# Optimization experiments

Measured on AMD Instinct MI355X. Metric: run time of the kernel, lower is better.

Reference implementation:

```python
import jax, jax.numpy as jnp
import numpy as np

N_NODES = 100000
N_EDGES = 1_600_000
IN_DIM, HID, OUT_DIM, N_BLOCKS = 963, 192, 3, 6


def spmm(src, dst, w, x):
    # sparse adj @ x, adj[dst, src] = w  (COO edge list)
    msgs = x[src] * w[:, None]                      # [E, F]
    return jax.ops.segment_sum(msgs, dst, num_segments=N_NODES)


def gconv(x, src, dst, ew, w, lw, b):
    # Pixel2Mesh GConv: adj @ (x @ W) + x @ W_loop + b
    return spmm(src, dst, ew, x @ w) + x @ lw + b


def setup_inputs() -> dict:
    key = jax.random.key(0)
    ks = jax.random.split(key, 13)
    s = 0.02  # small init scale to keep deep stack numerically tame
    return {
        "inputs": jax.random.normal(ks[0], (N_NODES, IN_DIM), jnp.float32),
        "edge_src": jax.random.randint(ks[1], (N_EDGES,), 0, N_NODES),
        "edge_dst": jax.random.randint(ks[2], (N_EDGES,), 0, N_NODES),
        "edge_weight": jax.random.uniform(ks[3], (N_EDGES,), jnp.float32) / 16.0,
        "w_in": jax.random.normal(ks[4], (IN_DIM, HID), jnp.float32) * s,
        "loop_in": jax.random.normal(ks[5], (IN_DIM, HID), jnp.float32) * s,
        "b_in": jnp.zeros((HID,), jnp.float32),
        "blocks_w": jax.random.normal(ks[6], (N_BLOCKS, 2, HID, HID), jnp.float32) * s,
        "blocks_loop": jax.random.normal(ks[7], (N_BLOCKS, 2, HID, HID), jnp.float32) * s,
        "blocks_b": jnp.zeros((N_BLOCKS, 2, HID), jnp.float32),
        "w_out": jax.random.normal(ks[8], (HID, OUT_DIM), jnp.float32) * s,
        "loop_out": jax.random.normal(ks[9], (HID, OUT_DIM), jnp.float32) * s,
        "b_out": jnp.zeros((OUT_DIM,), jnp.float32),
    }


def reference(inputs, edge_src, edge_dst, edge_weight, w_in, loop_in, b_in,
              blocks_w, blocks_loop, blocks_b, w_out, loop_out, b_out):
    x = gconv(inputs, edge_src, edge_dst, edge_weight, w_in, loop_in, b_in)

    def block(x, params):
        bw, bl, bb = params
        h = gconv(x, edge_src, edge_dst, edge_weight, bw[0], bl[0], bb[0])
        h = gconv(h, edge_src, edge_dst, edge_weight, bw[1], bl[1], bb[1])
        return (x + h) * 0.5, None

    x_cat, _ = jax.lax.scan(block, x, (blocks_w, blocks_loop, blocks_b))
    x_out = gconv(x_cat, edge_src, edge_dst, edge_weight, w_out, loop_out, b_out)
    return (x_out, x_cat)
```

## Files before the change

kernel.cpp:

```cpp
#include <hip/hip_runtime.h>
#include <cstdint>
#include <cstddef>

#define N_NODES 100000
#define N_EDGES 1600000
#define IN_DIM 963
#define HID 192
#define OUT_DIM 3

typedef _Float16 f16x8 __attribute__((ext_vector_type(8)));
typedef _Float16 f16x4 __attribute__((ext_vector_type(4)));
typedef float f32x4 __attribute__((ext_vector_type(4)));

__global__ void count_kernel(const int* __restrict__ dst, int* __restrict__ counts, int E) {
    int i = blockIdx.x * blockDim.x + threadIdx.x;
    if (i < E) atomicAdd(&counts[dst[i]], 1);
}

__global__ void scan_kernel(const int* __restrict__ counts, int* __restrict__ row_ptr, int n) {
    __shared__ int buf[1024];
    __shared__ int carry_s;
    int t = threadIdx.x;
    if (t == 0) { carry_s = 0; row_ptr[0] = 0; }
    __syncthreads();
    for (int base = 0; base < n; base += 1024) {
        int idx = base + t;
        int v = (idx < n) ? counts[idx] : 0;
        buf[t] = v;
        __syncthreads();
        for (int off = 1; off < 1024; off <<= 1) {
            int add = (t >= off) ? buf[t - off] : 0;
            __syncthreads();
            buf[t] += add;
            __syncthreads();
        }
        int carry = carry_s;
        if (idx < n) row_ptr[idx + 1] = carry + buf[t];
        __syncthreads();
        if (t == 1023) carry_s = carry + buf[1023];
        __syncthreads();
    }
}

__global__ void copy_cursor_kernel(const int* __restrict__ rp, int* __restrict__ cursor, int n) {
    int i = blockIdx.x * blockDim.x + threadIdx.x;
    if (i < n) cursor[i] = rp[i];
}

__global__ void scatter_kernel(const int* __restrict__ src, const int* __restrict__ dst,
                               const float* __restrict__ w, int* __restrict__ cursor,
                               int* __restrict__ csr_src, float* __restrict__ csr_w,
                               int* __restrict__ csr_eid, int E) {
    int i = blockIdx.x * blockDim.x + threadIdx.x;
    if (i < E) {
        int d = dst[i];
        int p = atomicAdd(&cursor[d], 1);
        csr_src[p] = src[i];
        csr_w[p] = w[i];
        csr_eid[p] = i;
    }
}

__global__ void sortrow_kernel(const int* __restrict__ rp, int* __restrict__ csr_src,
                               float* __restrict__ csr_w, int* __restrict__ csr_eid, int n) {
    int r = blockIdx.x * blockDim.x + threadIdx.x;
    if (r >= n) return;
    int s = rp[r], e = rp[r + 1];
    for (int i = s + 1; i < e; ++i) {
        int ke = csr_eid[i]; int ks = csr_src[i]; float kw = csr_w[i];
        int j = i - 1;
        while (j >= s && csr_eid[j] > ke) {
            csr_eid[j + 1] = csr_eid[j];
            csr_src[j + 1] = csr_src[j];
            csr_w[j + 1] = csr_w[j];
            --j;
        }
        csr_eid[j + 1] = ke; csr_src[j + 1] = ks; csr_w[j + 1] = kw;
    }
}

__global__ __launch_bounds__(256)
void trans_split(const float* __restrict__ W, const float* __restrict__ L,
                 int K, int Kp, _Float16* __restrict__ out_hi, _Float16* __restrict__ out_lo) {
    __shared__ float tile[32][33];
    const int n0 = blockIdx.x * 32, k0 = blockIdx.y * 32;
    const int tx = threadIdx.x, ty = threadIdx.y;
#pragma unroll
    for (int i = 0; i < 4; ++i) {
        int k = k0 + ty + i * 8;
        int n = n0 + tx;
        float v = 0.f;
        if (k < K) v = (n < HID) ? W[(size_t)k * HID + n] : L[(size_t)k * HID + (n - HID)];
        tile[ty + i * 8][tx] = v;
    }
    __syncthreads();
#pragma unroll
    for (int i = 0; i < 4; ++i) {
        int nl = ty + i * 8;
        int n = n0 + nl;
        int k = k0 + tx;
        float v = tile[tx][nl];
        _Float16 hi = (_Float16)v;
        _Float16 lo = (_Float16)(v - (float)hi);
        out_hi[(size_t)n * Kp + k] = hi;
        out_lo[(size_t)n * Kp + k] = lo;
    }
}

__global__ __launch_bounds__(256, 2)
void gemm_mfma(const float* __restrict__ X, int M, int Kx, int Kp,
               const _Float16* __restrict__ Wth, const _Float16* __restrict__ Wtl,
               const float* __restrict__ bias, const float* __restrict__ res,
               float* __restrict__ Hdst, float* __restrict__ Tdst) {
    __shared__ __align__(16) _Float16 Ah[4096];
    __shared__ __align__(16) _Float16 Al[4096];
    __shared__ __align__(16) _Float16 Bh[4096];
    __shared__ __align__(16) _Float16 Bl[4096];

    const int m0 = blockIdx.x * 128;
    const int bcol = blockIdx.y * 128;
    const int tid = threadIdx.x;
    const int lane = tid & 63;
    const int wave = tid >> 6;
    const int wr = wave >> 1, wc = wave & 1;

    const int sr = tid >> 1;
    const int sh = tid & 1;
    const int arow = m0 + sr;
    const bool arok = arow < M;
    const float* xrow = X + (size_t)(arok ? arow : 0) * Kx;

    const int bnl_lo = tid >> 2;
    const int bq = tid & 3;

    f32x4 pa[4];
    f16x8 pb[4];

    auto loadA = [&](int k0) {
        if (arok && (k0 + 32) <= Kx) {
            const float* p = xrow + k0 + sh * 16;
            pa[0] = *(const f32x4*)(p);
            pa[1] = *(const f32x4*)(p + 4);
            pa[2] = *(const f32x4*)(p + 8);
            pa[3] = *(const f32x4*)(p + 12);
        } else {
#pragma unroll
            for (int c = 0; c < 4; ++c) {
                f32x4 v = {0.f, 0.f, 0.f, 0.f};
#pragma unroll
                for (int j = 0; j < 4; ++j) {
                    int k = k0 + sh * 16 + c * 4 + j;
                    if (arok && k < Kx) v[j] = xrow[k];
                }
                pa[c] = v;
            }
        }
    };
    auto loadB = [&](int k0) {
#pragma unroll
        for (int it = 0; it < 4; ++it) {
            const _Float16* srcp = (it < 2) ? Wth : Wtl;
            int nl = (it & 1) * 64 + bnl_lo;
            pb[it] = *(const f16x8*)(srcp + (size_t)(bcol + nl) * Kp + k0 + bq * 8);
        }
    };
    auto stashA = [&]() {
#pragma unroll
        for (int c = 0; c < 2; ++c) {
            f16x8 hi, lo;
#pragma unroll
            for (int j = 0; j < 8; ++j) {
                int e = c * 8 + j;
                float x = pa[e >> 2][e & 3];
                _Float16 h = (_Float16)x;
                hi[j] = h;
                lo[j] = (_Float16)(x - (float)h);
            }
            int kg = sh * 2 + c;
            int off = (sr >> 4) * 512 + kg * 128 + ((sr & 15) ^ kg) * 8;
            *(f16x8*)&Ah[off] = hi;
            *(f16x8*)&Al[off] = lo;
        }
    };
    auto stashB = [&]() {
#pragma unroll
        for (int it = 0; it < 4; ++it) {
            int nl = (it & 1) * 64 + bnl_lo;
            int off = (nl >> 4) * 512 + bq * 128 + ((nl & 15) ^ bq) * 8;
            _Float16* dst = (it < 2) ? Bh : Bl;
            *(f16x8*)&dst[off] = pb[it];
        }
    };

    f32x4 acc[4][4];
#pragma unroll
    for (int i = 0; i < 4; ++i)
#pragma unroll
        for (int j = 0; j < 4; ++j)
            acc[i][j] = f32x4{0.f, 0.f, 0.f, 0.f};

    const int lro = (lane >> 4) * 128 + ((lane & 15) ^ (lane >> 4)) * 8;

    loadA(0); loadB(0);
    for (int k0 = 0; k0 < Kx; k0 += 32) {
        stashA(); stashB();
        __syncthreads();
        if (k0 + 32 < Kx) { loadA(k0 + 32); loadB(k0 + 32); }
        f16x8 ah[4], al[4], bh[4], bl[4];
#pragma unroll
        for (int i = 0; i < 4; ++i) {
            ah[i] = *(const f16x8*)&Ah[(wr * 4 + i) * 512 + lro];
            al[i] = *(const f16x8*)&Al[(wr * 4 + i) * 512 + lro];
            bh[i] = *(const f16x8*)&Bh[(wc * 4 + i) * 512 + lro];
            bl[i] = *(const f16x8*)&Bl[(wc * 4 + i) * 512 + lro];
        }
#pragma unroll
        for (int mi = 0; mi < 4; ++mi)
#pragma unroll
            for (int ni = 0; ni < 4; ++ni) {
                acc[mi][ni] = __builtin_amdgcn_mfma_f32_16x16x32_f16(ah[mi], bh[ni], acc[mi][ni], 0, 0, 0);
                acc[mi][ni] = __builtin_amdgcn_mfma_f32_16x16x32_f16(al[mi], bh[ni], acc[mi][ni], 0, 0, 0);
                acc[mi][ni] = __builtin_amdgcn_mfma_f32_16x16x32_f16(ah[mi], bl[ni], acc[mi][ni], 0, 0, 0);
            }
        __syncthreads();
    }

#pragma unroll
    for (int mi = 0; mi < 4; ++mi) {
        int rbase = m0 + wr * 64 + mi * 16 + ((lane >> 4) << 2);
#pragma unroll
        for (int ni = 0; ni < 4; ++ni) {
            int gc = bcol + wc * 64 + ni * 16 + (lane & 15);
            f32x4 v = acc[mi][ni];
            if (gc < HID) {
#pragma unroll
                for (int j = 0; j < 4; ++j) {
                    int row = rbase + j;
                    if (row < M) Hdst[(size_t)row * HID + gc] = v[j];
                }
            } else {
                int c = gc - HID;
                float bv = bias[c];
#pragma unroll
                for (int j = 0; j < 4; ++j) {
                    int row = rbase + j;
                    if (row < M) {
                        float t = v[j] + bv;
                        if (res != nullptr) t += res[(size_t)row * HID + c];
                        Tdst[(size_t)row * HID + c] = t;
                    }
                }
            }
        }
    }
}

__global__ __launch_bounds__(256)
void spmm_kernel(const int* __restrict__ rp, const int* __restrict__ csrc,
                 const float* __restrict__ cw, const float* __restrict__ Hm,
                 float* __restrict__ out, float scale) {
    int wid = (blockIdx.x * 256 + threadIdx.x) >> 6;
    int lane = threadIdx.x & 63;
    if (wid >= N_NODES) return;
    int s = rp[wid], e = rp[wid + 1];
    float a0 = 0.f, a1 = 0.f, a2 = 0.f;
    int i = s;
    for (; i + 1 < e; i += 2) {
        float w0 = cw[i], w1 = cw[i + 1];
        const float* h0 = Hm + (size_t)csrc[i] * HID;
        const float* h1 = Hm + (size_t)csrc[i + 1] * HID;
        float x00 = h0[lane], x01 = h0[64 + lane], x02 = h0[128 + lane];
        float x10 = h1[lane], x11 = h1[64 + lane], x12 = h1[128 + lane];
        a0 += w0 * x00; a1 += w0 * x01; a2 += w0 * x02;
        a0 += w1 * x10; a1 += w1 * x11; a2 += w1 * x12;
    }
    if (i < e) {
        float w = cw[i];
        const float* h = Hm + (size_t)csrc[i] * HID;
        a0 += w * h[lane];
        a1 += w * h[64 + lane];
        a2 += w * h[128 + lane];
    }
    float* o = out + (size_t)wid * HID;
    o[lane]       = scale * (o[lane] + a0);
    o[64 + lane]  = scale * (o[64 + lane] + a1);
    o[128 + lane] = scale * (o[128 + lane] + a2);
}

__global__ __launch_bounds__(256)
void out_gemm(const float* __restrict__ X, const float* __restrict__ Wout,
              const float* __restrict__ Lout, const float* __restrict__ bout,
              float* __restrict__ H3, float* __restrict__ T3) {
    __shared__ float Ws[HID * OUT_DIM];
    __shared__ float Ls[HID * OUT_DIM];
    int tid = threadIdx.x;
    for (int i = tid; i < HID * OUT_DIM; i += 256) { Ws[i] = Wout[i]; Ls[i] = Lout[i]; }
    __syncthreads();
    int n = blockIdx.x * 4 + (tid >> 6);
    int lane = tid & 63;
    if (n >= N_NODES) return;
    const float* x = X + (size_t)n * HID;
    float aw[3] = {0.f, 0.f, 0.f}, al[3] = {0.f, 0.f, 0.f};
#pragma unroll
    for (int p = 0; p < 3; ++p) {
        int k = p * 64 + lane;
        float xv = x[k];
#pragma unroll
        for (int c = 0; c < 3; ++c) {
            aw[c] += xv * Ws[k * 3 + c];
            al[c] += xv * Ls[k * 3 + c];
        }
    }
#pragma unroll
    for (int off = 32; off > 0; off >>= 1) {
#pragma unroll
        for (int c = 0; c < 3; ++c) {
            aw[c] += __shfl_down(aw[c], off, 64);
            al[c] += __shfl_down(al[c], off, 64);
        }
    }
    if (lane == 0) {
#pragma unroll
        for (int c = 0; c < 3; ++c) {
            H3[n * 3 + c] = aw[c];
            T3[n * 3 + c] = al[c] + bout[c];
        }
    }
}

__global__ __launch_bounds__(256)
void out_spmm(const int* __restrict__ rp, const int* __restrict__ csrc,
              const float* __restrict__ cw, const float* __restrict__ H3,
              const float* __restrict__ T3, float* __restrict__ out) {
    int n = blockIdx.x * blockDim.x + threadIdx.x;
    if (n >= N_NODES) return;
    int s = rp[n], e = rp[n + 1];
    float a0 = 0.f, a1 = 0.f, a2 = 0.f;
    for (int i = s; i < e; ++i) {
        float w = cw[i];
        int src = csrc[i];
        a0 += w * H3[src * 3 + 0];
        a1 += w * H3[src * 3 + 1];
        a2 += w * H3[src * 3 + 2];
    }
    out[n * 3 + 0] = a0 + T3[n * 3 + 0];
    out[n * 3 + 1] = a1 + T3[n * 3 + 1];
    out[n * 3 + 2] = a2 + T3[n * 3 + 2];
}

extern "C" void kernel_launch(void* const* d_in, const int* in_sizes, int n_in,
                              void* d_out, int out_size, void* d_ws, size_t ws_size,
                              hipStream_t stream) {
    const float* X0    = (const float*)d_in[0];
    const int*   esrc  = (const int*)d_in[1];
    const int*   edst  = (const int*)d_in[2];
    const float* ew    = (const float*)d_in[3];
    const float* w_in  = (const float*)d_in[4];
    const float* l_in  = (const float*)d_in[5];
    const float* b_in  = (const float*)d_in[6];
    const float* bw    = (const float*)d_in[7];
    const float* bl    = (const float*)d_in[8];
    const float* bb    = (const float*)d_in[9];
    const float* w_out = (const float*)d_in[10];
    const float* l_out = (const float*)d_in[11];
    const float* b_out = (const float*)d_in[12];

    char* ws = (char*)d_ws;
    size_t off = 0;
    auto alloc = [&](size_t bytes) -> void* {
        void* p = ws + off;
        off += (bytes + 255) & ~(size_t)255;
        return p;
    };
    float* Hbuf   = (float*)alloc(sizeof(float) * (size_t)N_NODES * HID);
    float* h1     = (float*)alloc(sizeof(float) * (size_t)N_NODES * HID);
    int*   counts = (int*)alloc(sizeof(int) * N_NODES);
    int*   rp     = (int*)alloc(sizeof(int) * (N_NODES + 1));
    int*   cursor = (int*)alloc(sizeof(int) * N_NODES);
    int*   csrc   = (int*)alloc(sizeof(int) * N_EDGES);
    float* cw     = (float*)alloc(sizeof(float) * N_EDGES);
    int*   ceid   = (int*)alloc(sizeof(int) * N_EDGES);
    float* H3     = (float*)alloc(sizeof(float) * (size_t)N_NODES * OUT_DIM);
    float* T3     = (float*)alloc(sizeof(float) * (size_t)N_NODES * OUT_DIM);
    const int KP0 = 992;
    _Float16* Wt0h = (_Float16*)alloc(sizeof(_Float16) * 384 * KP0);
    _Float16* Wt0l = (_Float16*)alloc(sizeof(_Float16) * 384 * KP0);
    _Float16* WtHh = (_Float16*)alloc(sizeof(_Float16) * 12 * 384 * HID);
    _Float16* WtHl = (_Float16*)alloc(sizeof(_Float16) * 12 * 384 * HID);

    float* xout = (float*)d_out;
    float* xcat = (float*)d_out + (size_t)N_NODES * OUT_DIM;

    trans_split<<<dim3(12, 31), dim3(32, 8), 0, stream>>>(w_in, l_in, IN_DIM, KP0, Wt0h, Wt0l);
    for (int l = 0; l < 12; ++l) {
        trans_split<<<dim3(12, 6), dim3(32, 8), 0, stream>>>(
            bw + (size_t)l * HID * HID, bl + (size_t)l * HID * HID, HID, HID,
            WtHh + (size_t)l * 384 * HID, WtHl + (size_t)l * 384 * HID);
    }

    hipMemsetAsync(counts, 0, sizeof(int) * N_NODES, stream);
    count_kernel<<<(N_EDGES + 255) / 256, 256, 0, stream>>>(edst, counts, N_EDGES);
    scan_kernel<<<1, 1024, 0, stream>>>(counts, rp, N_NODES);
    copy_cursor_kernel<<<(N_NODES + 255) / 256, 256, 0, stream>>>(rp, cursor, N_NODES);
    scatter_kernel<<<(N_EDGES + 255) / 256, 256, 0, stream>>>(esrc, edst, ew, cursor,
                                                              csrc, cw, ceid, N_EDGES);
    sortrow_kernel<<<(N_NODES + 255) / 256, 256, 0, stream>>>(rp, csrc, cw, ceid, N_NODES);

    dim3 gemm_grid((N_NODES + 127) / 128, 3);
    int spmm_blocks = (N_NODES * 64 + 255) / 256;

    gemm_mfma<<<gemm_grid, 256, 0, stream>>>(X0, N_NODES, IN_DIM, KP0, Wt0h, Wt0l,
                                             b_in, nullptr, Hbuf, xcat);
    spmm_kernel<<<spmm_blocks, 256, 0, stream>>>(rp, csrc, cw, Hbuf, xcat, 1.0f);

    for (int b = 0; b < 6; ++b) {
        int l0 = b * 2, l1 = b * 2 + 1;
        const float* B0 = bb + (size_t)l0 * HID;
        const float* B1 = bb + (size_t)l1 * HID;

        gemm_mfma<<<gemm_grid, 256, 0, stream>>>(xcat, N_NODES, HID, HID,
                                                 WtHh + (size_t)l0 * 384 * HID,
                                                 WtHl + (size_t)l0 * 384 * HID,
                                                 B0, nullptr, Hbuf, h1);
        spmm_kernel<<<spmm_blocks, 256, 0, stream>>>(rp, csrc, cw, Hbuf, h1, 1.0f);
        gemm_mfma<<<gemm_grid, 256, 0, stream>>>(h1, N_NODES, HID, HID,
                                                 WtHh + (size_t)l1 * 384 * HID,
                                                 WtHl + (size_t)l1 * 384 * HID,
                                                 B1, xcat, Hbuf, xcat);
        spmm_kernel<<<spmm_blocks, 256, 0, stream>>>(rp, csrc, cw, Hbuf, xcat, 0.5f);
    }

    out_gemm<<<(N_NODES + 3) / 4, 256, 0, stream>>>(xcat, w_out, l_out, b_out, H3, T3);
    out_spmm<<<(N_NODES + 255) / 256, 256, 0, stream>>>(rp, csrc, cw, H3, T3, xout);
}
```

Baseline: 4.516 ms.

## Compute all 384 output columns per GEMM block and unroll SpMM edges by four

Each GEMM block now has 512 threads (8 waves) and computes the full 384-wide [W | W_loop] output for a 128-row tile, so the three-way column grid is gone. Each activation tile is read from global memory and split into fp16 hi/lo once instead of three times. The LDS layout moves to a row-major swizzle and the main loop is restructured around a register prefetch. SpMM gathers four neighbour rows per iteration instead of two to raise memory-level parallelism. The costs are more LDS and accumulator registers per block, which lowers occupancy to one block per CU.

```diff
diff --git a/kernel.cpp b/kernel.cpp
--- a/kernel.cpp
+++ b/kernel.cpp
@@ -9,7 +9,6 @@
 #define OUT_DIM 3
 
 typedef _Float16 f16x8 __attribute__((ext_vector_type(8)));
-typedef _Float16 f16x4 __attribute__((ext_vector_type(4)));
 typedef float f32x4 __attribute__((ext_vector_type(4)));
 
 __global__ void count_kernel(const int* __restrict__ dst, int* __restrict__ counts, int E) {
@@ -107,140 +106,147 @@
     }
 }
 
-__global__ __launch_bounds__(256, 2)
+__global__ __launch_bounds__(512, 1)
 void gemm_mfma(const float* __restrict__ X, int M, int Kx, int Kp,
                const _Float16* __restrict__ Wth, const _Float16* __restrict__ Wtl,
                const float* __restrict__ bias, const float* __restrict__ res,
                float* __restrict__ Hdst, float* __restrict__ Tdst) {
     __shared__ __align__(16) _Float16 Ah[4096];
     __shared__ __align__(16) _Float16 Al[4096];
-    __shared__ __align__(16) _Float16 Bh[4096];
-    __shared__ __align__(16) _Float16 Bl[4096];
+    __shared__ __align__(16) _Float16 Bh[12288];
+    __shared__ __align__(16) _Float16 Bl[12288];
 
     const int m0 = blockIdx.x * 128;
-    const int bcol = blockIdx.y * 128;
     const int tid = threadIdx.x;
     const int lane = tid & 63;
     const int wave = tid >> 6;
-    const int wr = wave >> 1, wc = wave & 1;
-
-    const int sr = tid >> 1;
-    const int sh = tid & 1;
-    const int arow = m0 + sr;
+    const int wr = wave >> 2;
+    const int wc = wave & 3;
+
+    const int q  = tid >> 2;
+    const int kg = tid & 3;
+    const int xr = (kg ^ q ^ (q >> 2)) & 3;
+    const int arow = m0 + q;
     const bool arok = arow < M;
     const float* xrow = X + (size_t)(arok ? arow : 0) * Kx;
 
-    const int bnl_lo = tid >> 2;
-    const int bq = tid & 3;
-
-    f32x4 pa[4];
-    f16x8 pb[4];
+    float pa[8];
+    f16x8 pbh[3], pbl[3];
 
     auto loadA = [&](int k0) {
-        if (arok && (k0 + 32) <= Kx) {
-            const float* p = xrow + k0 + sh * 16;
-            pa[0] = *(const f32x4*)(p);
-            pa[1] = *(const f32x4*)(p + 4);
-            pa[2] = *(const f32x4*)(p + 8);
-            pa[3] = *(const f32x4*)(p + 12);
+        int kb = k0 + kg * 8;
+        if (arok && kb + 8 <= Kx) {
+            f32x4 v0 = *(const f32x4*)(xrow + kb);
+            f32x4 v1 = *(const f32x4*)(xrow + kb + 4);
+#pragma unroll
+            for (int j = 0; j < 4; ++j) { pa[j] = v0[j]; pa[4 + j] = v1[j]; }
         } else {
 #pragma unroll
-            for (int c = 0; c < 4; ++c) {
-                f32x4 v = {0.f, 0.f, 0.f, 0.f};
-#pragma unroll
-                for (int j = 0; j < 4; ++j) {
-                    int k = k0 + sh * 16 + c * 4 + j;
-                    if (arok && k < Kx) v[j] = xrow[k];
-                }
-                pa[c] = v;
-            }
+            for (int j = 0; j < 8; ++j)
+                pa[j] = (arok && kb + j < Kx) ? xrow[kb + j] : 0.f;
         }
     };
     auto loadB = [&](int k0) {
 #pragma unroll
-        for (int it = 0; it < 4; ++it) {
-            const _Float16* srcp = (it < 2) ? Wth : Wtl;
-            int nl = (it & 1) * 64 + bnl_lo;
-            pb[it] = *(const f16x8*)(srcp + (size_t)(bcol + nl) * Kp + k0 + bq * 8);
+        for (int c = 0; c < 3; ++c) {
+            size_t o = (size_t)(c * 128 + q) * Kp + k0 + kg * 8;
+            pbh[c] = *(const f16x8*)(Wth + o);
+            pbl[c] = *(const f16x8*)(Wtl + o);
         }
     };
-    auto stashA = [&]() {
-#pragma unroll
-        for (int c = 0; c < 2; ++c) {
-            f16x8 hi, lo;
-#pragma unroll
-            for (int j = 0; j < 8; ++j) {
-                int e = c * 8 + j;
-                float x = pa[e >> 2][e & 3];
-                _Float16 h = (_Float16)x;
-                hi[j] = h;
-                lo[j] = (_Float16)(x - (float)h);
-            }
-            int kg = sh * 2 + c;
-            int off = (sr >> 4) * 512 + kg * 128 + ((sr & 15) ^ kg) * 8;
-            *(f16x8*)&Ah[off] = hi;
-            *(f16x8*)&Al[off] = lo;
+    auto stash = [&]() {
+        f16x8 hi, lo;
+#pragma unroll
+        for (int j = 0; j < 8; ++j) {
+            float x = pa[j];
+            _Float16 h = (_Float16)x;
+            hi[j] = h;
+            lo[j] = (_Float16)(x - (float)h);
+        }
+        const int aoff = q * 64 + xr * 16;
+        *(f16x8*)((char*)Ah + aoff) = hi;
+        *(f16x8*)((char*)Al + aoff) = lo;
+#pragma unroll
+        for (int c = 0; c < 3; ++c) {
+            const int boff = (c * 128 + q) * 64 + xr * 16;
+            *(f16x8*)((char*)Bh + boff) = pbh[c];
+            *(f16x8*)((char*)Bl + boff) = pbl[c];
         }
     };
-    auto stashB = [&]() {
-#pragma unroll
-        for (int it = 0; it < 4; ++it) {
-            int nl = (it & 1) * 64 + bnl_lo;
-            int off = (nl >> 4) * 512 + bq * 128 + ((nl & 15) ^ bq) * 8;
-            _Float16* dst = (it < 2) ? Bh : Bl;
-            *(f16x8*)&dst[off] = pb[it];
-        }
-    };
-
-    f32x4 acc[4][4];
+
+    int a_off[4], b_off[6];
+#pragma unroll
+    for (int mi = 0; mi < 4; ++mi) {
+        int idx = wr * 64 + mi * 16 + (lane & 15);
+        a_off[mi] = idx * 64 + ((((lane >> 4)) ^ idx ^ (idx >> 2)) & 3) * 16;
+    }
+#pragma unroll
+    for (int ni = 0; ni < 6; ++ni) {
+        int idx = wc * 96 + ni * 16 + (lane & 15);
+        b_off[ni] = idx * 64 + ((((lane >> 4)) ^ idx ^ (idx >> 2)) & 3) * 16;
+    }
+
+    f32x4 acc[4][6];
 #pragma unroll
     for (int i = 0; i < 4; ++i)
 #pragma unroll
-        for (int j = 0; j < 4; ++j)
+        for (int j = 0; j < 6; ++j)
             acc[i][j] = f32x4{0.f, 0.f, 0.f, 0.f};
 
-    const int lro = (lane >> 4) * 128 + ((lane & 15) ^ (lane >> 4)) * 8;
-
+    const int nsteps = (Kx + 31) / 32;
     loadA(0); loadB(0);
-    for (int k0 = 0; k0 < Kx; k0 += 32) {
-        stashA(); stashB();
-        __syncthreads();
-        if (k0 + 32 < Kx) { loadA(k0 + 32); loadB(k0 + 32); }
-        f16x8 ah[4], al[4], bh[4], bl[4];
-#pragma unroll
-        for (int i = 0; i < 4; ++i) {
-            ah[i] = *(const f16x8*)&Ah[(wr * 4 + i) * 512 + lro];
-            al[i] = *(const f16x8*)&Al[(wr * 4 + i) * 512 + lro];
-            bh[i] = *(const f16x8*)&Bh[(wc * 4 + i) * 512 + lro];
-            bl[i] = *(const f16x8*)&Bl[(wc * 4 + i) * 512 + lro];
-        }
-#pragma unroll
-        for (int mi = 0; mi < 4; ++mi)
-#pragma unroll
-            for (int ni = 0; ni < 4; ++ni) {
-                acc[mi][ni] = __builtin_amdgcn_mfma_f32_16x16x32_f16(ah[mi], bh[ni], acc[mi][ni], 0, 0, 0);
-                acc[mi][ni] = __builtin_amdgcn_mfma_f32_16x16x32_f16(al[mi], bh[ni], acc[mi][ni], 0, 0, 0);
-                acc[mi][ni] = __builtin_amdgcn_mfma_f32_16x16x32_f16(ah[mi], bl[ni], acc[mi][ni], 0, 0, 0);
-            }
-        __syncthreads();
-    }
-
+    stash();
+    __syncthreads();
+
+    for (int s = 0; s < nsteps; ++s) {
+        const int k0 = s * 32;
+        const bool more = (s + 1) < nsteps;
+        if (more) { loadA(k0 + 32); loadB(k0 + 32); }
+
+        f16x8 ah[4], al[4];
+#pragma unroll
+        for (int mi = 0; mi < 4; ++mi) {
+            ah[mi] = *(const f16x8*)((char*)Ah + a_off[mi]);
+            al[mi] = *(const f16x8*)((char*)Al + a_off[mi]);
+        }
+#pragma unroll
+        for (int ni = 0; ni < 6; ++ni) {
+            f16x8 bh = *(const f16x8*)((char*)Bh + b_off[ni]);
+            f16x8 bl = *(const f16x8*)((char*)Bl + b_off[ni]);
+#pragma unroll
+            for (int mi = 0; mi < 4; ++mi)
+                acc[mi][ni] = __builtin_amdgcn_mfma_f32_16x16x32_f16(ah[mi], bh, acc[mi][ni], 0, 0, 0);
+#pragma unroll
+            for (int mi = 0; mi < 4; ++mi)
+                acc[mi][ni] = __builtin_amdgcn_mfma_f32_16x16x32_f16(al[mi], bh, acc[mi][ni], 0, 0, 0);
+#pragma unroll
+            for (int mi = 0; mi < 4; ++mi)
+                acc[mi][ni] = __builtin_amdgcn_mfma_f32_16x16x32_f16(ah[mi], bl, acc[mi][ni], 0, 0, 0);
+        }
+        if (more) {
+            __syncthreads();
+            stash();
+            __syncthreads();
+        }
+    }
+
+    const bool isH = (wc < 2);
 #pragma unroll
     for (int mi = 0; mi < 4; ++mi) {
-        int rbase = m0 + wr * 64 + mi * 16 + ((lane >> 4) << 2);
-#pragma unroll
-        for (int ni = 0; ni < 4; ++ni) {
-            int gc = bcol + wc * 64 + ni * 16 + (lane & 15);
+        const int rbase = m0 + wr * 64 + mi * 16 + ((lane >> 4) << 2);
+#pragma unroll
+        for (int ni = 0; ni < 6; ++ni) {
+            const int gc = wc * 96 + ni * 16 + (lane & 15);
             f32x4 v = acc[mi][ni];
-            if (gc < HID) {
+            if (isH) {
 #pragma unroll
                 for (int j = 0; j < 4; ++j) {
                     int row = rbase + j;
                     if (row < M) Hdst[(size_t)row * HID + gc] = v[j];
                 }
             } else {
-                int c = gc - HID;
-                float bv = bias[c];
+                const int c = gc - HID;
+                const float bv = bias[c];
 #pragma unroll
                 for (int j = 0; j < 4; ++j) {
                     int row = rbase + j;
@@ -265,16 +271,22 @@
     int s = rp[wid], e = rp[wid + 1];
     float a0 = 0.f, a1 = 0.f, a2 = 0.f;
     int i = s;
-    for (; i + 1 < e; i += 2) {
-        float w0 = cw[i], w1 = cw[i + 1];
+    for (; i + 3 < e; i += 4) {
+        float w0 = cw[i], w1 = cw[i + 1], w2 = cw[i + 2], w3 = cw[i + 3];
         const float* h0 = Hm + (size_t)csrc[i] * HID;
         const float* h1 = Hm + (size_t)csrc[i + 1] * HID;
+        const float* h2 = Hm + (size_t)csrc[i + 2] * HID;
+        const float* h3 = Hm + (size_t)csrc[i + 3] * HID;
         float x00 = h0[lane], x01 = h0[64 + lane], x02 = h0[128 + lane];
         float x10 = h1[lane], x11 = h1[64 + lane], x12 = h1[128 + lane];
+        float x20 = h2[lane], x21 = h2[64 + lane], x22 = h2[128 + lane];
+        float x30 = h3[lane], x31 = h3[64 + lane], x32 = h3[128 + lane];
         a0 += w0 * x00; a1 += w0 * x01; a2 += w0 * x02;
         a0 += w1 * x10; a1 += w1 * x11; a2 += w1 * x12;
-    }
-    if (i < e) {
+        a0 += w2 * x20; a1 += w2 * x21; a2 += w2 * x22;
+        a0 += w3 * x30; a1 += w3 * x31; a2 += w3 * x32;
+    }
+    for (; i < e; ++i) {
         float w = cw[i];
         const float* h = Hm + (size_t)csrc[i] * HID;
         a0 += w * h[lane];
@@ -406,11 +418,11 @@
                                                               csrc, cw, ceid, N_EDGES);
     sortrow_kernel<<<(N_NODES + 255) / 256, 256, 0, stream>>>(rp, csrc, cw, ceid, N_NODES);
 
-    dim3 gemm_grid((N_NODES + 127) / 128, 3);
-    int spmm_blocks = (N_NODES * 64 + 255) / 256;
-
-    gemm_mfma<<<gemm_grid, 256, 0, stream>>>(X0, N_NODES, IN_DIM, KP0, Wt0h, Wt0l,
-                                             b_in, nullptr, Hbuf, xcat);
+    const int gemm_blocks = (N_NODES + 127) / 128;
+    const int spmm_blocks = (N_NODES * 64 + 255) / 256;
+
+    gemm_mfma<<<gemm_blocks, 512, 0, stream>>>(X0, N_NODES, IN_DIM, KP0, Wt0h, Wt0l,
+                                               b_in, nullptr, Hbuf, xcat);
     spmm_kernel<<<spmm_blocks, 256, 0, stream>>>(rp, csrc, cw, Hbuf, xcat, 1.0f);
 
     for (int b = 0; b < 6; ++b) {
@@ -418,15 +430,15 @@
         const float* B0 = bb + (size_t)l0 * HID;
         const float* B1 = bb + (size_t)l1 * HID;
 
-        gemm_mfma<<<gemm_grid, 256, 0, stream>>>(xcat, N_NODES, HID, HID,
-                                                 WtHh + (size_t)l0 * 384 * HID,
-                                                 WtHl + (size_t)l0 * 384 * HID,
-                                                 B0, nullptr, Hbuf, h1);
+        gemm_mfma<<<gemm_blocks, 512, 0, stream>>>(xcat, N_NODES, HID, HID,
+                                                   WtHh + (size_t)l0 * 384 * HID,
+                                                   WtHl + (size_t)l0 * 384 * HID,
+                                                   B0, nullptr, Hbuf, h1);
         spmm_kernel<<<spmm_blocks, 256, 0, stream>>>(rp, csrc, cw, Hbuf, h1, 1.0f);
-        gemm_mfma<<<gemm_grid, 256, 0, stream>>>(h1, N_NODES, HID, HID,
-                                                 WtHh + (size_t)l1 * 384 * HID,
-                                                 WtHl + (size_t)l1 * 384 * HID,
-                                                 B1, xcat, Hbuf, xcat);
+        gemm_mfma<<<gemm_blocks, 512, 0, stream>>>(h1, N_NODES, HID, HID,
+                                                   WtHh + (size_t)l1 * 384 * HID,
+                                                   WtHl + (size_t)l1 * 384 * HID,
+                                                   B1, xcat, Hbuf, xcat);
         spmm_kernel<<<spmm_blocks, 256, 0, stream>>>(rp, csrc, cw, Hbuf, xcat, 0.5f);
     }
 
```

After: 5.217 ms. 15.5% more time.
